# Kernel tuning notes

Measured on AMD Instinct MI355X. Metric: run time of the kernel, lower is better.

Reference implementation:

```python
import jax, jax.numpy as jnp
import numpy as np

B, S, D = 2, 2048, 1024
H, DK, DV = 16, 64, 64
EPS = 1e-5
SQRT_DK = float(np.sqrt(DK))


def setup_inputs() -> dict:
    key = jax.random.key(0)
    ks = jax.random.split(key, 8)
    sc = 0.02
    return {
        "x": jax.random.normal(ks[0], (B, S, D), jnp.float32),
        "Wk": jax.random.normal(ks[1], (D, H * DK), jnp.float32) * sc,
        "bk": jnp.zeros((H * DK,), jnp.float32),
        "Wq": jax.random.normal(ks[2], (D, H * DK), jnp.float32) * sc,
        "bq": jnp.zeros((H * DK,), jnp.float32),
        "Wv": jax.random.normal(ks[3], (D, H * DV), jnp.float32) * sc,
        "bv": jnp.zeros((H * DV,), jnp.float32),
        "Wo": jax.random.normal(ks[4], (H * DV, D), jnp.float32) * sc,
        "bo": jnp.zeros((D,), jnp.float32),
        "gamma": jnp.ones((D,), jnp.float32),
        "beta": jnp.zeros((D,), jnp.float32),
    }


def reference(x, Wk, bk, Wq, bq, Wv, bv, Wo, bo, gamma, beta):
    b, s, d = x.shape
    # NOTE: original torch code reshapes (B, S, H*dk) directly to (B, H, S, dk)
    # without a transpose; we replicate that exact (non-standard) reshape.
    keys = (x @ Wk + bk).reshape(b, H, s, DK)
    queries = (x @ Wq + bq).reshape(b, H, s, DK)
    values = (x @ Wv + bv).reshape(b, H, s, DV)

    scores = jnp.einsum('bhqd,bhkd->bhqk', queries, keys) / SQRT_DK
    causal_mask = jnp.triu(jnp.ones((s, s), bool), k=1)  # True = masked
    scores = jnp.where(causal_mask[None, None], jnp.float32(-1e9), scores)
    attention = jax.nn.softmax(scores, axis=-1)

    context = jnp.einsum('bhqk,bhkd->bhqd', attention, values)
    context = context.reshape(b, s, H * DV)

    out = context @ Wo + bo  # dropout is identity at inference
    out = out + x            # residual connection

    mean = jnp.mean(out, axis=-1, keepdims=True)
    var = jnp.mean(jnp.square(out - mean), axis=-1, keepdims=True)
    return (out - mean) / jnp.sqrt(var + EPS) * gamma + beta
```

## Files before the change

kernel.cpp:

```cpp
#include <hip/hip_runtime.h>


typedef __attribute__((ext_vector_type(8))) __bf16 bf16x8;
typedef __attribute__((ext_vector_type(8))) unsigned short ushort8;
typedef __attribute__((ext_vector_type(4))) float f32x4;

static __device__ __forceinline__ unsigned short f2bf(float f) {
    unsigned u = __builtin_bit_cast(unsigned, f);
    u += 0x7fffu + ((u >> 16) & 1u);
    return (unsigned short)(u >> 16);
}

__global__ __launch_bounds__(256) void cast_kernel(const float* __restrict__ src,
                                                   unsigned short* __restrict__ dst, int n4) {
    int i = blockIdx.x * 256 + threadIdx.x;
    if (i >= n4) return;
    float4 v = ((const float4*)src)[i];
    ushort4 o;
    o.x = f2bf(v.x); o.y = f2bf(v.y); o.z = f2bf(v.z); o.w = f2bf(v.w);
    ((ushort4*)dst)[i] = o;
}

__global__ __launch_bounds__(256) void castT_kernel(const float* __restrict__ src,
                                                    unsigned short* __restrict__ dst) {
    __shared__ __align__(16) unsigned short t[64 * 68];
    const int tid = threadIdx.x;
    const int n0 = blockIdx.x * 64, k0 = blockIdx.y * 64;
    #pragma unroll
    for (int u = 0; u < 4; u++) {
        int e = u * 256 + tid;
        int r = e >> 4, c4 = (e & 15) * 4;
        float4 v = *(const float4*)(src + (k0 + r) * 1024 + n0 + c4);
        ushort4 o;
        o.x = f2bf(v.x); o.y = f2bf(v.y); o.z = f2bf(v.z); o.w = f2bf(v.w);
        *(ushort4*)(t + r * 68 + c4) = o;
    }
    __syncthreads();
    #pragma unroll
    for (int u = 0; u < 4; u++) {
        int e = u * 256 + tid;
        int rn = e >> 4, ck = (e & 15) * 4;
        ushort4 o;
        o.x = t[(ck + 0) * 68 + rn];
        o.y = t[(ck + 1) * 68 + rn];
        o.z = t[(ck + 2) * 68 + rn];
        o.w = t[(ck + 3) * 68 + rn];
        *(ushort4*)(dst + (n0 + rn) * 1024 + k0 + ck) = o;
    }
}

__global__ __launch_bounds__(256) void vtrans_kernel(const unsigned short* __restrict__ V,
                                                     unsigned short* __restrict__ VT) {
    __shared__ __align__(16) unsigned short t[64 * 68];
    const int tid = threadIdx.x;
    const int p0 = blockIdx.x * 64;
    const long base = (long)blockIdx.y * 131072;
    #pragma unroll
    for (int u = 0; u < 2; u++) {
        int e = u * 256 + tid;
        int r = e >> 3, c8 = (e & 7) * 8;
        ushort8 v = *(const ushort8*)(V + base + (long)(p0 + r) * 64 + c8);
        *(ushort8*)(t + r * 68 + c8) = v;
    }
    __syncthreads();
    #pragma unroll
    for (int u = 0; u < 4; u++) {
        int e = u * 256 + tid;
        int dv = e >> 4, pk = (e & 15) * 4;
        ushort4 o;
        o.x = t[(pk + 0) * 68 + dv];
        o.y = t[(pk + 1) * 68 + dv];
        o.z = t[(pk + 2) * 68 + dv];
        o.w = t[(pk + 3) * 68 + dv];
        *(ushort4*)(VT + base + (long)dv * 2048 + p0 + pk) = o;
    }
}

__global__ __launch_bounds__(256, 3) void gemm_kernel(
    const unsigned short* __restrict__ A,
    const unsigned short* __restrict__ Bt,
    const float* __restrict__ b0, const float* __restrict__ b1, const float* __restrict__ b2,
    unsigned short* __restrict__ outQ, unsigned short* __restrict__ outK,
    unsigned short* __restrict__ outV,
    float* __restrict__ outF, const float* __restrict__ resid, int mode)
{
    __shared__ __align__(16) unsigned short As[2][128 * 32];
    __shared__ __align__(16) unsigned short Bs[2][128 * 32];
    const int tid = threadIdx.x;
    const int lane = tid & 63, wave = tid >> 6;
    const int quad = lane >> 4, l16 = lane & 15;
    const int wm = wave >> 1, wn = wave & 1;
    const int row0 = blockIdx.y * 128, n0g = blockIdx.x * 128;

    const int sr = tid >> 2;
    const int sc = (tid & 3) * 8;
    const unsigned short* Ag0 = A + (size_t)(row0 + sr) * 1024 + sc;
    const unsigned short* Ag1 = A + (size_t)(row0 + 64 + sr) * 1024 + sc;
    const unsigned short* Bg0 = Bt + (size_t)(n0g + sr) * 1024 + sc;
    const unsigned short* Bg1 = Bt + (size_t)(n0g + 64 + sr) * 1024 + sc;

    {
        ushort8 a0 = *(const ushort8*)(Ag0);
        ushort8 a1 = *(const ushort8*)(Ag1);
        ushort8 bv0 = *(const ushort8*)(Bg0);
        ushort8 bv1 = *(const ushort8*)(Bg1);
        *(ushort8*)(As[0] + sr * 32 + sc) = a0;
        *(ushort8*)(As[0] + (64 + sr) * 32 + sc) = a1;
        *(ushort8*)(Bs[0] + sr * 32 + sc) = bv0;
        *(ushort8*)(Bs[0] + (64 + sr) * 32 + sc) = bv1;
    }
    __syncthreads();

    f32x4 acc[4][4] = {};
    #pragma unroll 2
    for (int it = 0; it < 32; ++it) {
        const int cur = it & 1;
        ushort8 na0, na1, nb0, nb1;
        if (it < 31) {
            const int k0 = (it + 1) * 32;
            na0 = *(const ushort8*)(Ag0 + k0);
            na1 = *(const ushort8*)(Ag1 + k0);
            nb0 = *(const ushort8*)(Bg0 + k0);
            nb1 = *(const ushort8*)(Bg1 + k0);
        }
        bf16x8 af[4], bfr[4];
        #pragma unroll
        for (int i = 0; i < 4; i++)
            af[i] = *(const bf16x8*)(As[cur] + (wm * 64 + i * 16 + l16) * 32 + quad * 8);
        #pragma unroll
        for (int j = 0; j < 4; j++)
            bfr[j] = *(const bf16x8*)(Bs[cur] + (wn * 64 + j * 16 + l16) * 32 + quad * 8);
        #pragma unroll
        for (int i = 0; i < 4; i++)
            #pragma unroll
            for (int j = 0; j < 4; j++)
                acc[i][j] = __builtin_amdgcn_mfma_f32_16x16x32_bf16(af[i], bfr[j], acc[i][j], 0, 0, 0);
        if (it < 31) {
            const int nxt = cur ^ 1;
            *(ushort8*)(As[nxt] + sr * 32 + sc) = na0;
            *(ushort8*)(As[nxt] + (64 + sr) * 32 + sc) = na1;
            *(ushort8*)(Bs[nxt] + sr * 32 + sc) = nb0;
            *(ushort8*)(Bs[nxt] + (64 + sr) * 32 + sc) = nb1;
            __syncthreads();
        }
    }

    if (mode == 0) {
        const int which = n0g >> 10;
        const float* bp = (which == 0) ? b0 : (which == 1) ? b1 : b2;
        unsigned short* op = (which == 0) ? outQ : (which == 1) ? outK : outV;
        #pragma unroll
        for (int i = 0; i < 4; i++)
            #pragma unroll
            for (int j = 0; j < 4; j++) {
                int c = (n0g + wn * 64 + j * 16 + l16) & 1023;
                float bj = bp[c];
                #pragma unroll
                for (int r = 0; r < 4; r++) {
                    int r_g = row0 + wm * 64 + i * 16 + quad * 4 + r;
                    op[(size_t)r_g * 1024 + c] = f2bf(acc[i][j][r] + bj);
                }
            }
    } else {
        #pragma unroll
        for (int i = 0; i < 4; i++)
            #pragma unroll
            for (int j = 0; j < 4; j++) {
                int c_g = n0g + wn * 64 + j * 16 + l16;
                float bj = b0[c_g];
                #pragma unroll
                for (int r = 0; r < 4; r++) {
                    int r_g = row0 + wm * 64 + i * 16 + quad * 4 + r;
                    size_t idx = (size_t)r_g * 1024 + c_g;
                    outF[idx] = acc[i][j][r] + bj + resid[idx];
                }
            }
    }
}

__global__ __launch_bounds__(256) void flash_kernel(
    const unsigned short* __restrict__ Q,
    const unsigned short* __restrict__ K,
    const unsigned short* __restrict__ VT,
    unsigned short* __restrict__ Ctx)
{
    __shared__ __align__(16) unsigned short Kt[128 * 72];
    __shared__ __align__(16) unsigned short Vt[64 * 136];
    __shared__ __align__(16) unsigned short Pt[4][16 * 140];
    const int tid = threadIdx.x;
    const int lane = tid & 63, wave = tid >> 6;
    const int quad = lane >> 4, l16 = lane & 15;
    const int qb = 31 - blockIdx.y;
    const int q0 = qb * 64;
    const long base = (long)blockIdx.x * 131072;

    bf16x8 qa[2];
    #pragma unroll
    for (int kk = 0; kk < 2; kk++)
        qa[kk] = *(const bf16x8*)(Q + base + (q0 + wave * 16 + l16) * 64 + kk * 32 + quad * 8);

    f32x4 o[4] = {};
    float l_part[4] = {0.f, 0.f, 0.f, 0.f};
    const int nt = (qb + 2) >> 1;

    for (int t = 0; t < nt; t++) {
        const int k0 = t * 128;
        #pragma unroll
        for (int u = 0; u < 4; u++) {
            int e = u * 256 + tid;
            int r = e >> 3, c = (e & 7) * 8;
            *(ushort8*)(Kt + r * 72 + c) = *(const ushort8*)(K + base + (long)(k0 + r) * 64 + c);
            int dv = e >> 4, kc = (e & 15) * 8;
            *(ushort8*)(Vt + dv * 136 + kc) = *(const ushort8*)(VT + base + (long)dv * 2048 + k0 + kc);
        }
        __syncthreads();

        f32x4 s[8];
        #pragma unroll
        for (int c = 0; c < 8; c++) {
            bf16x8 kb0 = *(const bf16x8*)(Kt + (c * 16 + l16) * 72 + quad * 8);
            bf16x8 kb1 = *(const bf16x8*)(Kt + (c * 16 + l16) * 72 + 32 + quad * 8);
            f32x4 a = {};
            a = __builtin_amdgcn_mfma_f32_16x16x32_bf16(qa[0], kb0, a, 0, 0, 0);
            a = __builtin_amdgcn_mfma_f32_16x16x32_bf16(qa[1], kb1, a, 0, 0, 0);
            s[c] = a;
        }
        const bool diag = (t == nt - 1);
        #pragma unroll
        for (int c = 0; c < 8; c++)
            #pragma unroll
            for (int r = 0; r < 4; r++) {
                float p = __expf(s[c][r] * 0.125f);
                if (diag) {
                    int kpos = k0 + c * 16 + l16;
                    int qpos = q0 + wave * 16 + quad * 4 + r;
                    p = (kpos > qpos) ? 0.f : p;
                }
                s[c][r] = p;
            }
        #pragma unroll
        for (int r = 0; r < 4; r++) {
            float t0 = (s[0][r] + s[1][r]) + (s[2][r] + s[3][r]);
            float t1 = (s[4][r] + s[5][r]) + (s[6][r] + s[7][r]);
            l_part[r] += t0 + t1;
        }
        unsigned short* pw = Pt[wave];
        #pragma unroll
        for (int c = 0; c < 8; c++)
            #pragma unroll
            for (int r = 0; r < 4; r++)
                pw[(quad * 4 + r) * 140 + c * 16 + l16] = f2bf(s[c][r]);
        bf16x8 pa[4];
        #pragma unroll
        for (int kk = 0; kk < 4; kk++) {
            const unsigned short* pr = pw + l16 * 140 + kk * 32 + quad * 8;
            ushort4 lo = *(const ushort4*)(pr);
            ushort4 hi = *(const ushort4*)(pr + 4);
            ushort8 u8;
            u8[0] = lo.x; u8[1] = lo.y; u8[2] = lo.z; u8[3] = lo.w;
            u8[4] = hi.x; u8[5] = hi.y; u8[6] = hi.z; u8[7] = hi.w;
            pa[kk] = __builtin_bit_cast(bf16x8, u8);
        }
        #pragma unroll
        for (int c2 = 0; c2 < 4; c2++)
            #pragma unroll
            for (int kk = 0; kk < 4; kk++) {
                bf16x8 vb = *(const bf16x8*)(Vt + (c2 * 16 + l16) * 136 + kk * 32 + quad * 8);
                o[c2] = __builtin_amdgcn_mfma_f32_16x16x32_bf16(pa[kk], vb, o[c2], 0, 0, 0);
            }
        __syncthreads();
    }

    #pragma unroll
    for (int r = 0; r < 4; r++) {
        float l = l_part[r];
        #pragma unroll
        for (int off = 1; off < 16; off <<= 1) l += __shfl_xor(l, off, 64);
        l_part[r] = 1.0f / l;
    }
    #pragma unroll
    for (int c2 = 0; c2 < 4; c2++)
        #pragma unroll
        for (int r = 0; r < 4; r++) {
            int row = q0 + wave * 16 + quad * 4 + r;
            Ctx[base + (long)row * 64 + c2 * 16 + l16] = f2bf(o[c2][r] * l_part[r]);
        }
}

__global__ __launch_bounds__(256) void ln_kernel(const float* __restrict__ inp,
                                                 const float* __restrict__ gamma,
                                                 const float* __restrict__ beta,
                                                 float* __restrict__ out)
{
    __shared__ float ssum[4], ssq[4];
    const int row = blockIdx.x;
    const int tid = threadIdx.x;
    float4 v = ((const float4*)(inp + (size_t)row * 1024))[tid];
    float s = v.x + v.y + v.z + v.w;
    float q = v.x * v.x + v.y * v.y + v.z * v.z + v.w * v.w;
    #pragma unroll
    for (int off = 32; off >= 1; off >>= 1) {
        s += __shfl_xor(s, off, 64);
        q += __shfl_xor(q, off, 64);
    }
    if ((tid & 63) == 0) { ssum[tid >> 6] = s; ssq[tid >> 6] = q; }
    __syncthreads();
    float ts = ssum[0] + ssum[1] + ssum[2] + ssum[3];
    float tq = ssq[0] + ssq[1] + ssq[2] + ssq[3];
    float mean = ts * (1.f / 1024.f);
    float var = tq * (1.f / 1024.f) - mean * mean;
    float rinv = rsqrtf(var + 1e-5f);
    float4 g = ((const float4*)gamma)[tid];
    float4 b = ((const float4*)beta)[tid];
    float4 o;
    o.x = (v.x - mean) * rinv * g.x + b.x;
    o.y = (v.y - mean) * rinv * g.y + b.y;
    o.z = (v.z - mean) * rinv * g.z + b.z;
    o.w = (v.w - mean) * rinv * g.w + b.w;
    ((float4*)(out + (size_t)row * 1024))[tid] = o;
}

extern "C" void kernel_launch(void* const* d_in, const int* in_sizes, int n_in,
                              void* d_out, int out_size, void* d_ws, size_t ws_size,
                              hipStream_t stream) {
    const float* x     = (const float*)d_in[0];
    const float* Wk    = (const float*)d_in[1];
    const float* bk    = (const float*)d_in[2];
    const float* Wq    = (const float*)d_in[3];
    const float* bq    = (const float*)d_in[4];
    const float* Wv    = (const float*)d_in[5];
    const float* bv    = (const float*)d_in[6];
    const float* Wo    = (const float*)d_in[7];
    const float* bo    = (const float*)d_in[8];
    const float* gamma = (const float*)d_in[9];
    const float* beta  = (const float*)d_in[10];
    float* out = (float*)d_out;

    char* ws = (char*)d_ws;
    unsigned short* xb    = (unsigned short*)(ws);
    unsigned short* WqkvT = (unsigned short*)(ws + (8ull << 20));
    unsigned short* WoT   = (unsigned short*)(ws + (14ull << 20));
    unsigned short* Qb    = (unsigned short*)(ws + (16ull << 20));
    unsigned short* Kb    = (unsigned short*)(ws + (24ull << 20));
    unsigned short* VbT   = (unsigned short*)(ws + (32ull << 20));
    unsigned short* Cb    = (unsigned short*)(ws + (40ull << 20));
    float* outp           = (float*)(ws + (48ull << 20));
    unsigned short* Vbn   = Cb;

    cast_kernel<<<4096, 256, 0, stream>>>(x, xb, 1048576);
    dim3 tgrid(16, 16);
    castT_kernel<<<tgrid, 256, 0, stream>>>(Wq, WqkvT);
    castT_kernel<<<tgrid, 256, 0, stream>>>(Wk, WqkvT + (1u << 20));
    castT_kernel<<<tgrid, 256, 0, stream>>>(Wv, WqkvT + (2u << 20));
    castT_kernel<<<tgrid, 256, 0, stream>>>(Wo, WoT);

    dim3 qkvgrid(24, 32);
    gemm_kernel<<<qkvgrid, 256, 0, stream>>>(xb, WqkvT, bq, bk, bv,
                                             Qb, Kb, Vbn, nullptr, nullptr, 0);

    dim3 vgrid(32, 32);
    vtrans_kernel<<<vgrid, 256, 0, stream>>>(Vbn, VbT);

    dim3 fgrid(32, 32);
    flash_kernel<<<fgrid, 256, 0, stream>>>(Qb, Kb, VbT, Cb);

    dim3 ogrid(8, 32);
    gemm_kernel<<<ogrid, 256, 0, stream>>>(Cb, WoT, bo, nullptr, nullptr,
                                           nullptr, nullptr, nullptr, outp, x, 1);

    ln_kernel<<<4096, 256, 0, stream>>>(outp, gamma, beta, out);
}
```

Measured before the change: 235.4 us.

## Prefetch next K/V tile into registers in flash kernel and fold softmax scale into Q

The flash attention loop now loads the next K/V tile from global memory into registers while the current tile's MFMAs run, then writes them to shared memory after the compute. This hides global-load latency behind compute. The 1/sqrt(dk) scale moves into the QKV projection epilogue so the exp skips a multiply, and launch bounds request 3 blocks per CU. The register prefetch raises register pressure, which may clash with the occupancy hint and cause spills. Scaling Q before bf16 rounding also slightly changes numerics.

```diff
diff --git a/kernel.cpp b/kernel.cpp
--- a/kernel.cpp
+++ b/kernel.cpp
@@ -149,6 +149,7 @@
         const int which = n0g >> 10;
         const float* bp = (which == 0) ? b0 : (which == 1) ? b1 : b2;
         unsigned short* op = (which == 0) ? outQ : (which == 1) ? outK : outV;
+        const float scl = (which == 0) ? 0.125f : 1.0f;
         #pragma unroll
         for (int i = 0; i < 4; i++)
             #pragma unroll
@@ -158,7 +159,7 @@
                 #pragma unroll
                 for (int r = 0; r < 4; r++) {
                     int r_g = row0 + wm * 64 + i * 16 + quad * 4 + r;
-                    op[(size_t)r_g * 1024 + c] = f2bf(acc[i][j][r] + bj);
+                    op[(size_t)r_g * 1024 + c] = f2bf((acc[i][j][r] + bj) * scl);
                 }
             }
     } else {
@@ -178,7 +179,7 @@
     }
 }
 
-__global__ __launch_bounds__(256) void flash_kernel(
+__global__ __launch_bounds__(256, 3) void flash_kernel(
     const unsigned short* __restrict__ Q,
     const unsigned short* __restrict__ K,
     const unsigned short* __restrict__ VT,
@@ -203,17 +204,30 @@
     float l_part[4] = {0.f, 0.f, 0.f, 0.f};
     const int nt = (qb + 2) >> 1;
 
+    #pragma unroll
+    for (int u = 0; u < 4; u++) {
+        int e = u * 256 + tid;
+        int r = e >> 3, c = (e & 7) * 8;
+        *(ushort8*)(Kt + r * 72 + c) = *(const ushort8*)(K + base + (long)r * 64 + c);
+        int dv = e >> 4, kc = (e & 15) * 8;
+        *(ushort8*)(Vt + dv * 136 + kc) = *(const ushort8*)(VT + base + (long)dv * 2048 + kc);
+    }
+    __syncthreads();
+
     for (int t = 0; t < nt; t++) {
+        ushort8 nk[4], nv[4];
+        if (t + 1 < nt) {
+            const int k1 = (t + 1) * 128;
+            #pragma unroll
+            for (int u = 0; u < 4; u++) {
+                int e = u * 256 + tid;
+                int r = e >> 3, c = (e & 7) * 8;
+                nk[u] = *(const ushort8*)(K + base + (long)(k1 + r) * 64 + c);
+                int dv = e >> 4, kc = (e & 15) * 8;
+                nv[u] = *(const ushort8*)(VT + base + (long)dv * 2048 + k1 + kc);
+            }
+        }
         const int k0 = t * 128;
-        #pragma unroll
-        for (int u = 0; u < 4; u++) {
-            int e = u * 256 + tid;
-            int r = e >> 3, c = (e & 7) * 8;
-            *(ushort8*)(Kt + r * 72 + c) = *(const ushort8*)(K + base + (long)(k0 + r) * 64 + c);
-            int dv = e >> 4, kc = (e & 15) * 8;
-            *(ushort8*)(Vt + dv * 136 + kc) = *(const ushort8*)(VT + base + (long)dv * 2048 + k0 + kc);
-        }
-        __syncthreads();
 
         f32x4 s[8];
         #pragma unroll
@@ -230,7 +244,7 @@
         for (int c = 0; c < 8; c++)
             #pragma unroll
             for (int r = 0; r < 4; r++) {
-                float p = __expf(s[c][r] * 0.125f);
+                float p = __expf(s[c][r]);
                 if (diag) {
                     int kpos = k0 + c * 16 + l16;
                     int qpos = q0 + wave * 16 + quad * 4 + r;
@@ -269,6 +283,17 @@
                 o[c2] = __builtin_amdgcn_mfma_f32_16x16x32_bf16(pa[kk], vb, o[c2], 0, 0, 0);
             }
         __syncthreads();
+        if (t + 1 < nt) {
+            #pragma unroll
+            for (int u = 0; u < 4; u++) {
+                int e = u * 256 + tid;
+                int r = e >> 3, c = (e & 7) * 8;
+                *(ushort8*)(Kt + r * 72 + c) = nk[u];
+                int dv = e >> 4, kc = (e & 15) * 8;
+                *(ushort8*)(Vt + dv * 136 + kc) = nv[u];
+            }
+            __syncthreads();
+        }
     }
 
     #pragma unroll
```

Measured after the change: 211.7 us. -10.1%, faster.
